# Performance work log

Hardware: AMD Instinct MI355X
Metric: run time of the kernel (lower is better)

## Reference

```python
import jax, jax.numpy as jnp
import numpy as np

MODS = ['linguistic', 'emotient', 'acoustic', 'image']
HID = {'linguistic': 128, 'emotient': 20, 'acoustic': 64, 'image': 128}
DIMS = {'linguistic': 300, 'emotient': 30, 'acoustic': 88, 'image': 1000}
B, T = 64, 512
TOTAL_HID = sum(HID[m] for m in MODS)  # 340
FUSE_HID = 64


def setup_inputs() -> dict:
    key = jax.random.key(0)
    ks = iter(jax.random.split(key, 64))
    inp = {}
    for mod in MODS:
        H, D = HID[mod], DIMS[mod]
        s = 1.0 / np.sqrt(H)
        inp[f'x_{mod}'] = jax.random.normal(next(ks), (B, T, D), jnp.float32)
        inp[f'present_{mod}'] = jax.random.randint(next(ks), (B, T), 0, 2).astype(jnp.int32)
        inp[f'W_ih_{mod}'] = jax.random.uniform(next(ks), (4 * H, D), jnp.float32, -s, s)
        inp[f'W_hh_{mod}'] = jax.random.uniform(next(ks), (4 * H, H), jnp.float32, -s, s)
        inp[f'b_ih_{mod}'] = jax.random.uniform(next(ks), (4 * H,), jnp.float32, -s, s)
        inp[f'b_hh_{mod}'] = jax.random.uniform(next(ks), (4 * H,), jnp.float32, -s, s)
    inp['seq_length'] = jax.random.randint(next(ks), (B,), 1, T + 1).astype(jnp.int32)
    valid = (jnp.arange(T)[None, :] < inp['seq_length'][:, None])
    inp['lstm_masks'] = valid.astype(jnp.float32)[:, :, None]
    s1 = 1.0 / np.sqrt(TOTAL_HID)
    inp['fuse_W1'] = jax.random.uniform(next(ks), (FUSE_HID, TOTAL_HID), jnp.float32, -s1, s1)
    inp['fuse_b1'] = jax.random.uniform(next(ks), (FUSE_HID,), jnp.float32, -s1, s1)
    s2 = 1.0 / np.sqrt(FUSE_HID)
    inp['fuse_W2'] = jax.random.uniform(next(ks), (1, FUSE_HID), jnp.float32, -s2, s2)
    inp['fuse_b2'] = jax.random.uniform(next(ks), (1,), jnp.float32, -s2, s2)
    return inp


def _lstm_scan(x, present, W_ih, W_hh, b_ih, b_hh):
    # x: [B,T,D], present: [B,T] in {0,1}. Carries (h,c) when not present (async arrival).
    Bn, Tn, _ = x.shape
    H = W_hh.shape[1]
    xg = jnp.einsum('btd,gd->btg', x, W_ih) + b_ih  # [B,T,4H] batched input GEMM

    def step(carry, inp):
        h, c = carry
        xg_t, p_t = inp  # [B,4H], [B]
        g = xg_t + h @ W_hh.T + b_hh
        i, f, gg, o = jnp.split(g, 4, axis=-1)
        i, f, o = jax.nn.sigmoid(i), jax.nn.sigmoid(f), jax.nn.sigmoid(o)
        gg = jnp.tanh(gg)
        c_new = f * c + i * gg
        h_new = o * jnp.tanh(c_new)
        p = p_t[:, None].astype(h.dtype)
        h2 = p * h_new + (1.0 - p) * h
        c2 = p * c_new + (1.0 - p) * c
        return (h2, c2), h2

    init = (jnp.zeros((Bn, H), x.dtype), jnp.zeros((Bn, H), x.dtype))
    _, hs = jax.lax.scan(step, init, (jnp.swapaxes(xg, 0, 1), present.T))
    return jnp.swapaxes(hs, 0, 1)  # [B,T,H]


def reference(x_linguistic, x_emotient, x_acoustic, x_image,
              present_linguistic, present_emotient, present_acoustic, present_image,
              W_ih_linguistic, W_hh_linguistic, b_ih_linguistic, b_hh_linguistic,
              W_ih_emotient, W_hh_emotient, b_ih_emotient, b_hh_emotient,
              W_ih_acoustic, W_hh_acoustic, b_ih_acoustic, b_hh_acoustic,
              W_ih_image, W_hh_image, b_ih_image, b_hh_image,
              seq_length, lstm_masks, fuse_W1, fuse_b1, fuse_W2, fuse_b2):
    xs = {'linguistic': x_linguistic, 'emotient': x_emotient, 'acoustic': x_acoustic, 'image': x_image}
    pres = {'linguistic': present_linguistic, 'emotient': present_emotient,
            'acoustic': present_acoustic, 'image': present_image}
    Wih = {'linguistic': W_ih_linguistic, 'emotient': W_ih_emotient, 'acoustic': W_ih_acoustic, 'image': W_ih_image}
    Whh = {'linguistic': W_hh_linguistic, 'emotient': W_hh_emotient, 'acoustic': W_hh_acoustic, 'image': W_hh_image}
    bih = {'linguistic': b_ih_linguistic, 'emotient': b_ih_emotient, 'acoustic': b_ih_acoustic, 'image': b_ih_image}
    bhh = {'linguistic': b_hh_linguistic, 'emotient': b_hh_emotient, 'acoustic': b_hh_acoustic, 'image': b_hh_image}
    hs = [_lstm_scan(xs[m], pres[m], Wih[m], Whh[m], bih[m], bhh[m]) for m in MODS]
    h = jnp.concatenate(hs, axis=-1)  # [B,T,340]
    # padded timesteps past seq_length are zeros in the original (zeros appended)
    valid = (jnp.arange(h.shape[1])[None, :] < seq_length[:, None]).astype(h.dtype)
    h = h * valid[:, :, None]
    out = h @ fuse_W1.T + fuse_b1  # Dropout is identity at inference
    out = out @ fuse_W2.T + fuse_b2
    return out * lstm_masks
```

## Files before the change

kernel.cpp:

```cpp
#include <hip/hip_runtime.h>
#include <stdint.h>

typedef __bf16 bf16_t;
typedef _Float16 fp16_t;
typedef bf16_t bf16x8 __attribute__((ext_vector_type(8)));
typedef fp16_t fp16x4 __attribute__((ext_vector_type(4)));
typedef float f32x4 __attribute__((ext_vector_type(4)));

#define LOG2E 1.44269504088896340736f

__device__ __forceinline__ float sigm(float x) {
    return __builtin_amdgcn_rcpf(1.f + __builtin_amdgcn_exp2f(-LOG2E * x));
}
__device__ __forceinline__ float tanh_(float x) {
    return 1.f - 2.f * __builtin_amdgcn_rcpf(1.f + __builtin_amdgcn_exp2f((2.f * LOG2E) * x));
}

template <int CTRL>
__device__ __forceinline__ float dpp_add(float x) {
    int perm = __builtin_amdgcn_update_dpp(0, __float_as_int(x), CTRL, 0xF, 0xF, true);
    return x + __int_as_float(perm);
}
__device__ __forceinline__ float red16(float x) {
    x = dpp_add<0xB1>(x);
    x = dpp_add<0x4E>(x);
    x = dpp_add<0x124>(x);
    x = dpp_add<0x128>(x);
    return x;
}

__device__ __forceinline__ fp16x4 ldg_coh8(const fp16_t* p) {
    unsigned long long v = __hip_atomic_load((const unsigned long long*)p,
                                             __ATOMIC_RELAXED, __HIP_MEMORY_SCOPE_AGENT);
    union { unsigned long long u; fp16x4 f; } c; c.u = v; return c.f;
}
__device__ __forceinline__ fp16_t ldg_coh2(const fp16_t* p) {
    unsigned short v = __hip_atomic_load((const unsigned short*)p,
                                         __ATOMIC_RELAXED, __HIP_MEMORY_SCOPE_AGENT);
    union { unsigned short u; fp16_t f; } c; c.u = v; return c.f;
}

__device__ __forceinline__ void gate_chunk(const int* fp, int need, int cn,
                                           int tid, int* wml, int& wmr) {
    if (cn < wmr) return;
    if (tid == 0) {
        while (__hip_atomic_load(fp + cn, __ATOMIC_RELAXED, __HIP_MEMORY_SCOPE_AGENT) < need)
            __builtin_amdgcn_s_sleep(2);
        int ah = cn + 16; if (ah > 127) ah = 127;
        int nw = (__hip_atomic_load(fp + ah, __ATOMIC_RELAXED, __HIP_MEMORY_SCOPE_AGENT) >= need)
                     ? ah + 1 : cn + 1;
        *wml = nw;
    }
    __syncthreads();
    wmr = *wml;
}

__global__ void prep_fuse(const float* __restrict__ W1, const float* __restrict__ b1,
                          const float* __restrict__ W2, const float* __restrict__ b2,
                          float* __restrict__ v) {
    int u = threadIdx.x;
    if (u < 340) {
        float s = 0.f;
        for (int j = 0; j < 64; j++) s += W2[j] * W1[j * 340 + u];
        v[u] = s;
    } else if (u == 340) {
        float s = 0.f;
        for (int j = 0; j < 64; j++) s += W2[j] * b1[j];
        v[340] = s + b2[0];
    }
}

struct ModGemm {
    const float* x; const float* w; const float* bih; const float* bhh; fp16_t* xg;
    int D; int KB; int N4; int hshift;
};
struct ModRec {
    const float* whh; const int* present; const fp16_t* xg;
    int N4; int voff;
};
struct MegaArgs {
    ModGemm gm[4];
    int slot_mi[11]; int slot_nb[11];
    ModRec rm[4];
    const float* vvec;
    float* s_out;
    int* flags;
    int need[4];
};

__device__ void gemm_body(const ModGemm mg, int nb, int bm, int mi,
                          int* __restrict__ flags, int tid,
                          bf16_t* sAh, bf16_t* sAl, bf16_t* sB) {
    const int ncol0 = nb << 7;
    const int w = tid >> 6, l = tid & 63, lm = l & 15, q = l >> 4;
    const int wm = w & 3, wn = w >> 2;
    const int D = mg.D, N4 = mg.N4;
    const int ra = tid >> 1, ca = (tid & 1) << 4;
    const int rb = tid >> 2, cb = (tid & 3) << 3;

    f32x4 acc[4][4];
#pragma unroll
    for (int a = 0; a < 4; a++)
#pragma unroll
        for (int b = 0; b < 4; b++) acc[a][b] = 0.f;

    for (int kb = 0; kb < mg.KB; kb++) {
        const int k0 = kb << 5;
        {
            long row = (long)(bm << 8) + ra;
            int tt = (int)(row >> 6), bb = (int)(row & 63);
            const float* base = mg.x + ((size_t)bb * 512 + tt) * D;
            const float* src = base + k0 + ca;
            union { bf16_t e[16]; bf16x8 v[2]; } uh, ul;
            if (k0 + ca + 16 <= D) {
#pragma unroll
                for (int j = 0; j < 16; j += 2) {
                    float2 f = *(const float2*)(src + j);
                    bf16_t h0 = (bf16_t)f.x, h1 = (bf16_t)f.y;
                    uh.e[j] = h0; uh.e[j + 1] = h1;
                    ul.e[j] = (bf16_t)(f.x - (float)h0);
                    ul.e[j + 1] = (bf16_t)(f.y - (float)h1);
                }
            } else {
#pragma unroll
                for (int j = 0; j < 16; j++) {
                    int k = k0 + ca + j;
                    float fv = (k < D) ? base[k] : 0.f;
                    bf16_t h0 = (bf16_t)fv;
                    uh.e[j] = h0; ul.e[j] = (bf16_t)(fv - (float)h0);
                }
            }
            *(bf16x8*)&sAh[ra * 40 + ca] = uh.v[0];
            *(bf16x8*)&sAh[ra * 40 + ca + 8] = uh.v[1];
            *(bf16x8*)&sAl[ra * 40 + ca] = ul.v[0];
            *(bf16x8*)&sAl[ra * 40 + ca + 8] = ul.v[1];
        }
        {
            int wrow = ncol0 + rb;
            bool vr = wrow < N4;
            const float* src = mg.w + (long)wrow * D + k0 + cb;
            union { bf16_t e[8]; bf16x8 v; } ub;
            if (vr && (k0 + cb + 8 <= D)) {
#pragma unroll
                for (int j = 0; j < 8; j += 2) {
                    float2 f = *(const float2*)(src + j);
                    ub.e[j] = (bf16_t)f.x; ub.e[j + 1] = (bf16_t)f.y;
                }
            } else {
#pragma unroll
                for (int j = 0; j < 8; j++) {
                    int k = k0 + cb + j;
                    ub.e[j] = (vr && k < D) ? (bf16_t)mg.w[(long)wrow * D + k] : (bf16_t)0.f;
                }
            }
            *(bf16x8*)&sB[rb * 40 + cb] = ub.v;
        }
        __syncthreads();
        bf16x8 ah[4], al[4];
#pragma unroll
        for (int mt = 0; mt < 4; mt++) {
            int row = (wm << 6) + (mt << 4) + lm;
            ah[mt] = *(const bf16x8*)&sAh[row * 40 + (q << 3)];
            al[mt] = *(const bf16x8*)&sAl[row * 40 + (q << 3)];
        }
#pragma unroll
        for (int nt = 0; nt < 4; nt++) {
            bf16x8 bfv = *(const bf16x8*)&sB[((wn << 6) + (nt << 4) + lm) * 40 + (q << 3)];
#pragma unroll
            for (int mt = 0; mt < 4; mt++) {
                acc[mt][nt] = __builtin_amdgcn_mfma_f32_16x16x32_bf16(ah[mt], bfv, acc[mt][nt], 0, 0, 0);
                acc[mt][nt] = __builtin_amdgcn_mfma_f32_16x16x32_bf16(al[mt], bfv, acc[mt][nt], 0, 0, 0);
            }
        }
        __syncthreads();
    }
#pragma unroll
    for (int nt = 0; nt < 4; nt++) {
        int col = ncol0 + (wn << 6) + (nt << 4) + lm;
        if (col >= N4) continue;
        float bias = mg.bih[col] + mg.bhh[col];
        int colout = mg.hshift ? ((col & ((1 << mg.hshift) - 1)) << 2) | (col >> mg.hshift) : col;
#pragma unroll
        for (int mt = 0; mt < 4; mt++) {
#pragma unroll
            for (int r = 0; r < 4; r++) {
                long row = (long)(bm << 8) + (wm << 6) + (mt << 4) + (q << 2) + r;
                mg.xg[(size_t)row * N4 + colout] = (fp16_t)(acc[mt][nt][r] + bias);
            }
        }
    }
    __syncthreads();
    if (tid == 0) {
        __hip_atomic_fetch_add(&flags[mi * 128 + bm], 1, __ATOMIC_RELEASE,
                               __HIP_MEMORY_SCOPE_AGENT);
    }
}

template <int H>
__device__ __forceinline__ void rec_step(
    int t, bool act, int w, int lm, int q, int b0,
    const bf16x8 (&wf)[4][H / 32], float vv,
    fp16x4 (&xvs)[4], const fp16_t* const (&px)[4], size_t tstride,
    float (&h_st)[4], float (&c_st)[4],
    const unsigned (&pw)[4], const bf16_t* __restrict__ hbR,
    bf16_t* __restrict__ hbW, float* __restrict__ s_out) {
    constexpr int KT = H / 32, Hp = H + 8;
    if (act) {
        bf16x8 af[KT];
#pragma unroll
        for (int kt = 0; kt < KT; kt++)
            af[kt] = *(const bf16x8*)&hbR[lm * Hp + (kt << 5) + (q << 3)];
        f32x4 accv[4];
#pragma unroll
        for (int g = 0; g < 4; g++)
#pragma unroll
            for (int r = 0; r < 4; r++)
                accv[g][r] = (float)xvs[r][g];
        int tn = t + 4;
        if (tn < 512) {
#pragma unroll
            for (int r = 0; r < 4; r++)
                xvs[r] = ldg_coh8(px[r] + (size_t)tn * tstride);
        }
#pragma unroll
        for (int kt = 0; kt < KT; kt++)
#pragma unroll
            for (int g = 0; g < 4; g++)
                accv[g] = __builtin_amdgcn_mfma_f32_16x16x32_bf16(af[kt], wf[g][kt], accv[g], 0, 0, 0);
        float cr[4];
#pragma unroll
        for (int r = 0; r < 4; r++) {
            float gi = sigm(accv[0][r]);
            float gf = sigm(accv[1][r]);
            float gg = tanh_(accv[2][r]);
            float go = sigm(accv[3][r]);
            float cn = gf * c_st[r] + gi * gg;
            float hn = go * tanh_(cn);
            bool pb = ((pw[r] >> (t & 31)) & 1u) != 0u;
            h_st[r] = pb ? hn : h_st[r];
            c_st[r] = pb ? cn : c_st[r];
            cr[r] = h_st[r] * vv;
        }
        const int u = (w << 4) + lm;
#pragma unroll
        for (int r = 0; r < 4; r++)
            hbW[((q << 2) + r) * Hp + u] = (bf16_t)h_st[r];
#pragma unroll
        for (int r = 0; r < 4; r++)
            cr[r] = red16(cr[r]);
        if (lm == 0) {
#pragma unroll
            for (int r = 0; r < 4; r++)
                s_out[(size_t)((w << 6) + b0 + (q << 2) + r) * 512 + t] = cr[r];
        }
    }
    __syncthreads();
}

template <int H>
__device__ void rec_mfma(const ModRec M, int grp, float* __restrict__ s_out,
                         const float* __restrict__ vvec,
                         const int* __restrict__ flagp, int need,
                         unsigned* presw, bf16_t* hb0, bf16_t* hb1, int* wml, int tid) {
    constexpr int KT = H / 32, TPG = H / 16, Hp = H + 8;
    const int N4 = 4 * H;
    const int w = tid >> 6, l = tid & 63, lm = l & 15, q = l >> 4;
    const int b0 = grp << 4;
    const bool act = (w < TPG);

    for (int i = tid; i < 16 * Hp; i += 512) { hb0[i] = (bf16_t)0.f; hb1[i] = (bf16_t)0.f; }
    for (int i = tid; i < 256; i += 512) {
        const int* ps = M.present + ((b0 + (i >> 4)) << 9) + ((i & 15) << 5);
        unsigned bits = 0u;
#pragma unroll
        for (int j = 0; j < 32; j++) bits |= (unsigned)(ps[j] != 0) << j;
        presw[i] = bits;
    }

    bf16x8 wf[4][KT];
    float vv = 0.f;
    const int u = (w << 4) + lm;
    if (act) {
#pragma unroll
        for (int g = 0; g < 4; g++) {
            int n = g * H + u;
#pragma unroll
            for (int kt = 0; kt < KT; kt++) {
                int k = (kt << 5) + (q << 3);
                const float* sp_ = M.whh + (long)n * H + k;
                float4 f0 = *(const float4*)sp_;
                float4 f1 = *(const float4*)(sp_ + 4);
                union { bf16_t e[8]; bf16x8 v; } uu;
                uu.e[0] = (bf16_t)f0.x; uu.e[1] = (bf16_t)f0.y;
                uu.e[2] = (bf16_t)f0.z; uu.e[3] = (bf16_t)f0.w;
                uu.e[4] = (bf16_t)f1.x; uu.e[5] = (bf16_t)f1.y;
                uu.e[6] = (bf16_t)f1.z; uu.e[7] = (bf16_t)f1.w;
                wf[g][kt] = uu.v;
            }
        }
        vv = vvec[M.voff + u];
    }
    const fp16_t* px[4];
#pragma unroll
    for (int r = 0; r < 4; r++)
        px[r] = M.xg + (size_t)(b0 + (q << 2) + r) * N4 + (u << 2);
    const size_t tstride = (size_t)64 * N4;

    int wmr = 0;
    gate_chunk(flagp, need, 0, tid, wml, wmr);

    fp16x4 xv[4][4];
    if (act) {
#pragma unroll
        for (int s = 0; s < 4; s++)
#pragma unroll
            for (int r = 0; r < 4; r++)
                xv[s][r] = ldg_coh8(px[r] + (size_t)s * tstride);
    }
    float h_st[4] = {0, 0, 0, 0}, c_st[4] = {0, 0, 0, 0};
    unsigned pw[4] = {0, 0, 0, 0};
    __syncthreads();

    for (int t0 = 0; t0 < 512; t0 += 4) {
        int cn = (t0 >> 2) + 1;
        if (cn < 128) gate_chunk(flagp, need, cn, tid, wml, wmr);
        if ((t0 & 31) == 0 && act) {
            int wd = t0 >> 5;
#pragma unroll
            for (int r = 0; r < 4; r++)
                pw[r] = presw[(((q << 2) + r) << 4) + wd];
        }
        rec_step<H>(t0 + 0, act, w, lm, q, b0, wf, vv, xv[0], px, tstride, h_st, c_st, pw, hb0, hb1, s_out);
        rec_step<H>(t0 + 1, act, w, lm, q, b0, wf, vv, xv[1], px, tstride, h_st, c_st, pw, hb1, hb0, s_out);
        rec_step<H>(t0 + 2, act, w, lm, q, b0, wf, vv, xv[2], px, tstride, h_st, c_st, pw, hb0, hb1, s_out);
        rec_step<H>(t0 + 3, act, w, lm, q, b0, wf, vv, xv[3], px, tstride, h_st, c_st, pw, hb1, hb0, s_out);
    }
}

__device__ void rec_emot(const ModRec M, int grp, float* __restrict__ s_out,
                         const float* __restrict__ vvec,
                         const int* __restrict__ flagp, int need,
                         float* presf, float* gbuf , float* he ,
                         int* wml, int tid) {
    const int b0 = grp << 4;
    for (int i = tid; i < 16 * 21; i += 512) he[i] = 0.f;
    for (int i = tid; i < 16 * 512; i += 512)
        presf[i] = (float)M.present[((b0 + (i >> 9)) << 9) + (i & 511)];
    const int bl = tid >> 5;
    const int j0 = tid & 31;
    const bool has2 = (j0 < 16);
    float wr0[20], wr1[20], wr2[20];
#pragma unroll
    for (int k = 0; k < 20; k++) {
        wr0[k] = M.whh[j0 * 20 + k];
        wr1[k] = M.whh[(j0 + 32) * 20 + k];
        wr2[k] = has2 ? M.whh[(j0 + 64) * 20 + k] : 0.f;
    }
    const int b2 = tid / 20, u2 = tid % 20;
    const bool p2 = (tid < 320);
    float c_st = 0.f, h_st = 0.f;
    const fp16_t* px = M.xg + (size_t)(b0 + bl) * 80;

    int wmr = 0;
    gate_chunk(flagp, need, 0, tid, wml, wmr);

    fp16_t e0[4], e1[4], e2[4];
#pragma unroll
    for (int s = 0; s < 4; s++) {
        const fp16_t* p = px + (size_t)s * 5120;
        e0[s] = ldg_coh2(p + j0);
        e1[s] = ldg_coh2(p + j0 + 32);
        e2[s] = has2 ? ldg_coh2(p + j0 + 64) : (fp16_t)0.f;
    }
    __syncthreads();

    for (int t0 = 0; t0 < 512; t0 += 4) {
        int cn = (t0 >> 2) + 1;
        if (cn < 128) gate_chunk(flagp, need, cn, tid, wml, wmr);
#pragma unroll
        for (int s = 0; s < 4; s++) {
            int t = t0 + s;
            float g0 = (float)e0[s];
            float g1 = (float)e1[s];
            float g2 = has2 ? (float)e2[s] : 0.f;
            int tn = t + 4;
            if (tn < 512) {
                const fp16_t* p = px + (size_t)tn * 5120;
                e0[s] = ldg_coh2(p + j0);
                e1[s] = ldg_coh2(p + j0 + 32);
                if (has2) e2[s] = ldg_coh2(p + j0 + 64);
            }
#pragma unroll
            for (int k = 0; k < 20; k++) {
                float hv = he[bl * 21 + k];
                g0 += wr0[k] * hv; g1 += wr1[k] * hv; g2 += wr2[k] * hv;
            }
            gbuf[bl * 81 + j0] = g0;
            gbuf[bl * 81 + j0 + 32] = g1;
            if (has2) gbuf[bl * 81 + j0 + 64] = g2;
            __syncthreads();
            if (p2) {
                float gi = sigm(gbuf[b2 * 81 + u2]);
                float gf = sigm(gbuf[b2 * 81 + u2 + 20]);
                float gg = tanh_(gbuf[b2 * 81 + u2 + 40]);
                float go = sigm(gbuf[b2 * 81 + u2 + 60]);
                float cn2 = gf * c_st + gi * gg;
                float hn = go * tanh_(cn2);
                float p = presf[b2 * 512 + t];
                bool pb = (p != 0.f);
                h_st = pb ? hn : h_st;
                c_st = pb ? cn2 : c_st;
                he[b2 * 21 + u2] = h_st;
            }
            __syncthreads();
            if (tid < 16) {
                float ssum = 0.f;
#pragma unroll
                for (int uu = 0; uu < 20; uu++) ssum += he[tid * 21 + uu] * vvec[M.voff + uu];
                s_out[((b0 + tid) << 9) + t] = ssum;
            }
        }
    }
}

__global__ __launch_bounds__(512) void mega(MegaArgs A) {
    __shared__ __align__(16) char smem[51712];
    const int tid = threadIdx.x;
    const int bid = blockIdx.x;
    if (bid < 16) {
        __builtin_amdgcn_s_setprio(3);
        float*    presf = (float*)smem;
        bf16_t*   hb0   = (bf16_t*)(smem + 32768);
        bf16_t*   hb1   = (bf16_t*)(smem + 37120);
        float*    gbuf  = (float*)(smem + 41472);
        float*    he    = (float*)(smem + 46656);
        unsigned* presw = (unsigned*)(smem + 48000);
        int*      wml   = (int*)(smem + 49024);
        const int mi = bid >> 2, grp = bid & 3;
        const ModRec M = A.rm[mi];
        const int* flagp = A.flags + mi * 128;
        const int need = A.need[mi];
        float* s_out = A.s_out + (size_t)mi * 8 * 64 * 512;
        if (mi == 1)      rec_emot(M, grp, s_out, A.vvec, flagp, need, presf, gbuf, he, wml, tid);
        else if (mi == 2) rec_mfma<64>(M, grp, s_out, A.vvec, flagp, need, presw, hb0, hb1, wml, tid);
        else              rec_mfma<128>(M, grp, s_out, A.vvec, flagp, need, presw, hb0, hb1, wml, tid);
    } else {
        bf16_t* sAh = (bf16_t*)smem;
        bf16_t* sAl = (bf16_t*)(smem + 20480);
        bf16_t* sB  = (bf16_t*)(smem + 40960);
        int e = bid - 16;
        int x = e & 7;
        int k = e >> 3;
        int bmi = (k / 11) * 8 + x;
        int slot = k % 11;
        int mi = A.slot_mi[slot];
        gemm_body(A.gm[mi], A.slot_nb[slot], bmi, mi, A.flags, tid, sAh, sAl, sB);
    }
}

__global__ void fuse_out(const float* __restrict__ sp, const float* __restrict__ v,
                         const float* __restrict__ masks, float* __restrict__ out) {
    int i = threadIdx.x + blockIdx.x * 256;
    float c0 = v[340];
    float s = 0.f;
#pragma unroll
    for (int w = 0; w < 8; w++) s += sp[(size_t)w * 32768 + i];
    s += sp[(size_t)8 * 32768 + i];
#pragma unroll
    for (int w = 16; w < 20; w++) s += sp[(size_t)w * 32768 + i];
#pragma unroll
    for (int w = 24; w < 32; w++) s += sp[(size_t)w * 32768 + i];
    out[i] = masks[i] * (s + c0);
}

extern "C" void kernel_launch(void* const* d_in, const int* in_sizes, int n_in,
                              void* d_out, int out_size, void* d_ws, size_t ws_size,
                              hipStream_t stream) {
    const float* xL = (const float*)d_in[0];
    const int*   pL = (const int*)d_in[1];
    const float* WihL = (const float*)d_in[2];
    const float* WhhL = (const float*)d_in[3];
    const float* bihL = (const float*)d_in[4];
    const float* bhhL = (const float*)d_in[5];
    const float* xE = (const float*)d_in[6];
    const int*   pE = (const int*)d_in[7];
    const float* WihE = (const float*)d_in[8];
    const float* WhhE = (const float*)d_in[9];
    const float* bihE = (const float*)d_in[10];
    const float* bhhE = (const float*)d_in[11];
    const float* xA = (const float*)d_in[12];
    const int*   pA = (const int*)d_in[13];
    const float* WihA = (const float*)d_in[14];
    const float* WhhA = (const float*)d_in[15];
    const float* bihA = (const float*)d_in[16];
    const float* bhhA = (const float*)d_in[17];
    const float* xI = (const float*)d_in[18];
    const int*   pI = (const int*)d_in[19];
    const float* WihI = (const float*)d_in[20];
    const float* WhhI = (const float*)d_in[21];
    const float* bihI = (const float*)d_in[22];
    const float* bhhI = (const float*)d_in[23];
    const float* masks = (const float*)d_in[25];
    const float* fW1 = (const float*)d_in[26];
    const float* fb1 = (const float*)d_in[27];
    const float* fW2 = (const float*)d_in[28];
    const float* fb2 = (const float*)d_in[29];

    char* ws = (char*)d_ws;
    float* v     = (float*)ws;
    int*   flags = (int*)(ws + 4096);
    float* spart = (float*)(ws + (1 << 16));
    fp16_t* xgL = (fp16_t*)(ws + (1 << 16) + (4 << 20));
    fp16_t* xgE = xgL + (size_t)32768 * 512;
    fp16_t* xgA = xgE + (size_t)32768 * 80;
    fp16_t* xgI = xgA + (size_t)32768 * 256;

    prep_fuse<<<dim3(1), dim3(512), 0, stream>>>(fW1, fb1, fW2, fb2, v);
    hipMemsetAsync(flags, 0, 4 * 128 * sizeof(int), stream);

    MegaArgs A;
    A.gm[0] = {xL, WihL, bihL, bhhL, xgL, 300,  10, 512, 7};
    A.gm[1] = {xE, WihE, bihE, bhhE, xgE, 30,   1,  80,  0};
    A.gm[2] = {xA, WihA, bihA, bhhA, xgA, 88,   3,  256, 6};
    A.gm[3] = {xI, WihI, bihI, bhhI, xgI, 1000, 32, 512, 7};
    const int mi_tab[11] = {3, 3, 3, 3, 0, 0, 0, 0, 2, 2, 1};
    const int nb_tab[11] = {0, 1, 2, 3, 0, 1, 2, 3, 0, 1, 0};
    for (int i = 0; i < 11; i++) { A.slot_mi[i] = mi_tab[i]; A.slot_nb[i] = nb_tab[i]; }
    A.rm[0] = {WhhL, pL, xgL, 512, 0};
    A.rm[1] = {WhhE, pE, xgE, 80,  128};
    A.rm[2] = {WhhA, pA, xgA, 256, 148};
    A.rm[3] = {WhhI, pI, xgI, 512, 212};
    A.vvec = v;
    A.s_out = spart;
    A.flags = flags;
    A.need[0] = 4; A.need[1] = 1; A.need[2] = 2; A.need[3] = 4;

    mega<<<dim3(16 + 128 * 11), dim3(512), 0, stream>>>(A);

    fuse_out<<<dim3(128), dim3(256), 0, stream>>>(spart, v, masks, (float*)d_out);
}
```

Baseline: 917.8 us.

## Run emotient LSTM recurrence on MFMA path by padding hidden size to 32

Replaces the scalar FP32 emotient recurrence (hidden 20) with the shared MFMA-based rec_mfma<32> path. W_hh is padded to 32 units per gate in a prep kernel, the input-gate buffer is widened to 128 columns with a gate-interleaved layout, and padded columns are written as zero. This removes the per-step syncthreads-heavy scalar loop and shrinks shared memory use, at the cost of wasted work on padded lanes. The fuse_out reduction now sums all partial slots written by the emotient wavefronts.

Result: slower. 954.3 us (+4.0%).

```diff
diff --git a/kernel.cpp b/kernel.cpp
--- a/kernel.cpp
+++ b/kernel.cpp
@@ -33,11 +33,6 @@
     unsigned long long v = __hip_atomic_load((const unsigned long long*)p,
                                              __ATOMIC_RELAXED, __HIP_MEMORY_SCOPE_AGENT);
     union { unsigned long long u; fp16x4 f; } c; c.u = v; return c.f;
-}
-__device__ __forceinline__ fp16_t ldg_coh2(const fp16_t* p) {
-    unsigned short v = __hip_atomic_load((const unsigned short*)p,
-                                         __ATOMIC_RELAXED, __HIP_MEMORY_SCOPE_AGENT);
-    union { unsigned short u; fp16_t f; } c; c.u = v; return c.f;
 }
 
 __device__ __forceinline__ void gate_chunk(const int* fp, int need, int cn,
@@ -57,7 +52,8 @@
 
 __global__ void prep_fuse(const float* __restrict__ W1, const float* __restrict__ b1,
                           const float* __restrict__ W2, const float* __restrict__ b2,
-                          float* __restrict__ v) {
+                          const float* __restrict__ whhE,
+                          float* __restrict__ v, float* __restrict__ we32) {
     int u = threadIdx.x;
     if (u < 340) {
         float s = 0.f;
@@ -68,15 +64,20 @@
         for (int j = 0; j < 64; j++) s += W2[j] * b1[j];
         v[340] = s + b2[0];
     }
+    for (int i = u; i < 4096; i += 512) {
+        int n = i >> 5, k = i & 31;
+        int g = n >> 5, uu = n & 31;
+        we32[i] = (uu < 20 && k < 20) ? whhE[(g * 20 + uu) * 20 + k] : 0.f;
+    }
 }
 
 struct ModGemm {
     const float* x; const float* w; const float* bih; const float* bhh; fp16_t* xg;
-    int D; int KB; int N4; int hshift;
+    int D; int KB; int N4; int hshift; int nW;
 };
 struct ModRec {
     const float* whh; const int* present; const fp16_t* xg;
-    int N4; int voff;
+    int voff; int vlim;
 };
 struct MegaArgs {
     ModGemm gm[4];
@@ -94,7 +95,7 @@
     const int ncol0 = nb << 7;
     const int w = tid >> 6, l = tid & 63, lm = l & 15, q = l >> 4;
     const int wm = w & 3, wn = w >> 2;
-    const int D = mg.D, N4 = mg.N4;
+    const int D = mg.D, N4 = mg.N4, nW = mg.nW;
     const int ra = tid >> 1, ca = (tid & 1) << 4;
     const int rb = tid >> 2, cb = (tid & 3) << 3;
 
@@ -137,7 +138,7 @@
         }
         {
             int wrow = ncol0 + rb;
-            bool vr = wrow < N4;
+            bool vr = wrow < nW;
             const float* src = mg.w + (long)wrow * D + k0 + cb;
             union { bf16_t e[8]; bf16x8 v; } ub;
             if (vr && (k0 + cb + 8 <= D)) {
@@ -178,14 +179,19 @@
     for (int nt = 0; nt < 4; nt++) {
         int col = ncol0 + (wn << 6) + (nt << 4) + lm;
         if (col >= N4) continue;
-        float bias = mg.bih[col] + mg.bhh[col];
-        int colout = mg.hshift ? ((col & ((1 << mg.hshift) - 1)) << 2) | (col >> mg.hshift) : col;
+        bool real = col < nW;
+        float bias = real ? (mg.bih[col] + mg.bhh[col]) : 0.f;
+        int colout;
+        if (mg.hshift) colout = ((col & ((1 << mg.hshift) - 1)) << 2) | (col >> mg.hshift);
+        else if (real) colout = ((col % 20) << 2) | (col / 20);
+        else           colout = col;
 #pragma unroll
         for (int mt = 0; mt < 4; mt++) {
 #pragma unroll
             for (int r = 0; r < 4; r++) {
                 long row = (long)(bm << 8) + (wm << 6) + (mt << 4) + (q << 2) + r;
-                mg.xg[(size_t)row * N4 + colout] = (fp16_t)(acc[mt][nt][r] + bias);
+                float val = real ? (acc[mt][nt][r] + bias) : 0.f;
+                mg.xg[(size_t)row * N4 + colout] = (fp16_t)val;
             }
         }
     }
@@ -298,7 +304,7 @@
                 wf[g][kt] = uu.v;
             }
         }
-        vv = vvec[M.voff + u];
+        vv = (u < M.vlim) ? vvec[M.voff + u] : 0.f;
     }
     const fp16_t* px[4];
 #pragma unroll
@@ -334,92 +340,6 @@
         rec_step<H>(t0 + 1, act, w, lm, q, b0, wf, vv, xv[1], px, tstride, h_st, c_st, pw, hb1, hb0, s_out);
         rec_step<H>(t0 + 2, act, w, lm, q, b0, wf, vv, xv[2], px, tstride, h_st, c_st, pw, hb0, hb1, s_out);
         rec_step<H>(t0 + 3, act, w, lm, q, b0, wf, vv, xv[3], px, tstride, h_st, c_st, pw, hb1, hb0, s_out);
-    }
-}
-
-__device__ void rec_emot(const ModRec M, int grp, float* __restrict__ s_out,
-                         const float* __restrict__ vvec,
-                         const int* __restrict__ flagp, int need,
-                         float* presf, float* gbuf , float* he ,
-                         int* wml, int tid) {
-    const int b0 = grp << 4;
-    for (int i = tid; i < 16 * 21; i += 512) he[i] = 0.f;
-    for (int i = tid; i < 16 * 512; i += 512)
-        presf[i] = (float)M.present[((b0 + (i >> 9)) << 9) + (i & 511)];
-    const int bl = tid >> 5;
-    const int j0 = tid & 31;
-    const bool has2 = (j0 < 16);
-    float wr0[20], wr1[20], wr2[20];
-#pragma unroll
-    for (int k = 0; k < 20; k++) {
-        wr0[k] = M.whh[j0 * 20 + k];
-        wr1[k] = M.whh[(j0 + 32) * 20 + k];
-        wr2[k] = has2 ? M.whh[(j0 + 64) * 20 + k] : 0.f;
-    }
-    const int b2 = tid / 20, u2 = tid % 20;
-    const bool p2 = (tid < 320);
-    float c_st = 0.f, h_st = 0.f;
-    const fp16_t* px = M.xg + (size_t)(b0 + bl) * 80;
-
-    int wmr = 0;
-    gate_chunk(flagp, need, 0, tid, wml, wmr);
-
-    fp16_t e0[4], e1[4], e2[4];
-#pragma unroll
-    for (int s = 0; s < 4; s++) {
-        const fp16_t* p = px + (size_t)s * 5120;
-        e0[s] = ldg_coh2(p + j0);
-        e1[s] = ldg_coh2(p + j0 + 32);
-        e2[s] = has2 ? ldg_coh2(p + j0 + 64) : (fp16_t)0.f;
-    }
-    __syncthreads();
-
-    for (int t0 = 0; t0 < 512; t0 += 4) {
-        int cn = (t0 >> 2) + 1;
-        if (cn < 128) gate_chunk(flagp, need, cn, tid, wml, wmr);
-#pragma unroll
-        for (int s = 0; s < 4; s++) {
-            int t = t0 + s;
-            float g0 = (float)e0[s];
-            float g1 = (float)e1[s];
-            float g2 = has2 ? (float)e2[s] : 0.f;
-            int tn = t + 4;
-            if (tn < 512) {
-                const fp16_t* p = px + (size_t)tn * 5120;
-                e0[s] = ldg_coh2(p + j0);
-                e1[s] = ldg_coh2(p + j0 + 32);
-                if (has2) e2[s] = ldg_coh2(p + j0 + 64);
-            }
-#pragma unroll
-            for (int k = 0; k < 20; k++) {
-                float hv = he[bl * 21 + k];
-                g0 += wr0[k] * hv; g1 += wr1[k] * hv; g2 += wr2[k] * hv;
-            }
-            gbuf[bl * 81 + j0] = g0;
-            gbuf[bl * 81 + j0 + 32] = g1;
-            if (has2) gbuf[bl * 81 + j0 + 64] = g2;
-            __syncthreads();
-            if (p2) {
-                float gi = sigm(gbuf[b2 * 81 + u2]);
-                float gf = sigm(gbuf[b2 * 81 + u2 + 20]);
-                float gg = tanh_(gbuf[b2 * 81 + u2 + 40]);
-                float go = sigm(gbuf[b2 * 81 + u2 + 60]);
-                float cn2 = gf * c_st + gi * gg;
-                float hn = go * tanh_(cn2);
-                float p = presf[b2 * 512 + t];
-                bool pb = (p != 0.f);
-                h_st = pb ? hn : h_st;
-                c_st = pb ? cn2 : c_st;
-                he[b2 * 21 + u2] = h_st;
-            }
-            __syncthreads();
-            if (tid < 16) {
-                float ssum = 0.f;
-#pragma unroll
-                for (int uu = 0; uu < 20; uu++) ssum += he[tid * 21 + uu] * vvec[M.voff + uu];
-                s_out[((b0 + tid) << 9) + t] = ssum;
-            }
-        }
     }
 }
 
@@ -429,19 +349,16 @@
     const int bid = blockIdx.x;
     if (bid < 16) {
         __builtin_amdgcn_s_setprio(3);
-        float*    presf = (float*)smem;
-        bf16_t*   hb0   = (bf16_t*)(smem + 32768);
-        bf16_t*   hb1   = (bf16_t*)(smem + 37120);
-        float*    gbuf  = (float*)(smem + 41472);
-        float*    he    = (float*)(smem + 46656);
-        unsigned* presw = (unsigned*)(smem + 48000);
-        int*      wml   = (int*)(smem + 49024);
+        bf16_t*   hb0   = (bf16_t*)smem;
+        bf16_t*   hb1   = (bf16_t*)(smem + 4352);
+        unsigned* presw = (unsigned*)(smem + 8704);
+        int*      wml   = (int*)(smem + 9728);
         const int mi = bid >> 2, grp = bid & 3;
         const ModRec M = A.rm[mi];
         const int* flagp = A.flags + mi * 128;
         const int need = A.need[mi];
         float* s_out = A.s_out + (size_t)mi * 8 * 64 * 512;
-        if (mi == 1)      rec_emot(M, grp, s_out, A.vvec, flagp, need, presf, gbuf, he, wml, tid);
+        if (mi == 1)      rec_mfma<32>(M, grp, s_out, A.vvec, flagp, need, presw, hb0, hb1, wml, tid);
         else if (mi == 2) rec_mfma<64>(M, grp, s_out, A.vvec, flagp, need, presw, hb0, hb1, wml, tid);
         else              rec_mfma<128>(M, grp, s_out, A.vvec, flagp, need, presw, hb0, hb1, wml, tid);
     } else {
@@ -464,8 +381,7 @@
     float c0 = v[340];
     float s = 0.f;
 #pragma unroll
-    for (int w = 0; w < 8; w++) s += sp[(size_t)w * 32768 + i];
-    s += sp[(size_t)8 * 32768 + i];
+    for (int w = 0; w < 10; w++) s += sp[(size_t)w * 32768 + i];
 #pragma unroll
     for (int w = 16; w < 20; w++) s += sp[(size_t)w * 32768 + i];
 #pragma unroll
@@ -509,27 +425,28 @@
     char* ws = (char*)d_ws;
     float* v     = (float*)ws;
     int*   flags = (int*)(ws + 4096);
+    float* we32  = (float*)(ws + 8192);
     float* spart = (float*)(ws + (1 << 16));
     fp16_t* xgL = (fp16_t*)(ws + (1 << 16) + (4 << 20));
     fp16_t* xgE = xgL + (size_t)32768 * 512;
-    fp16_t* xgA = xgE + (size_t)32768 * 80;
+    fp16_t* xgA = xgE + (size_t)32768 * 128;
     fp16_t* xgI = xgA + (size_t)32768 * 256;
 
-    prep_fuse<<<dim3(1), dim3(512), 0, stream>>>(fW1, fb1, fW2, fb2, v);
+    prep_fuse<<<dim3(1), dim3(512), 0, stream>>>(fW1, fb1, fW2, fb2, WhhE, v, we32);
     hipMemsetAsync(flags, 0, 4 * 128 * sizeof(int), stream);
 
     MegaArgs A;
-    A.gm[0] = {xL, WihL, bihL, bhhL, xgL, 300,  10, 512, 7};
-    A.gm[1] = {xE, WihE, bihE, bhhE, xgE, 30,   1,  80,  0};
-    A.gm[2] = {xA, WihA, bihA, bhhA, xgA, 88,   3,  256, 6};
-    A.gm[3] = {xI, WihI, bihI, bhhI, xgI, 1000, 32, 512, 7};
+    A.gm[0] = {xL, WihL, bihL, bhhL, xgL, 300,  10, 512, 7, 512};
+    A.gm[1] = {xE, WihE, bihE, bhhE, xgE, 30,   1,  128, 0, 80};
+    A.gm[2] = {xA, WihA, bihA, bhhA, xgA, 88,   3,  256, 6, 256};
+    A.gm[3] = {xI, WihI, bihI, bhhI, xgI, 1000, 32, 512, 7, 512};
     const int mi_tab[11] = {3, 3, 3, 3, 0, 0, 0, 0, 2, 2, 1};
     const int nb_tab[11] = {0, 1, 2, 3, 0, 1, 2, 3, 0, 1, 0};
     for (int i = 0; i < 11; i++) { A.slot_mi[i] = mi_tab[i]; A.slot_nb[i] = nb_tab[i]; }
-    A.rm[0] = {WhhL, pL, xgL, 512, 0};
-    A.rm[1] = {WhhE, pE, xgE, 80,  128};
-    A.rm[2] = {WhhA, pA, xgA, 256, 148};
-    A.rm[3] = {WhhI, pI, xgI, 512, 212};
+    A.rm[0] = {WhhL, pL, xgL, 0,   128};
+    A.rm[1] = {we32, pE, xgE, 128, 20};
+    A.rm[2] = {WhhA, pA, xgA, 148, 64};
+    A.rm[3] = {WhhI, pI, xgI, 212, 128};
     A.vvec = v;
     A.s_out = spart;
     A.flags = flags;
```
